# Kernel optimization log

Hardware: AMD Instinct MI355X
Metric: run time of the kernel (lower is better)

The kernel has to match this reference:

```python
import jax, jax.numpy as jnp
import numpy as np

B, S, D = 2, 2048, 2048
HQ, HKV, HD = 16, 8, 128
F = 8192
V = 32000
L = 2
SW = 512
SOFTCAP = 50.0
THETA = 10000.0
EPS = 1e-6
LAYER_TYPES = ("sliding_attention", "full_attention")
SCALE = HD ** -0.5


def _rms_norm(x, w):
    # Gemma-style RMSNorm: fp32 compute, (1 + weight) scale
    x32 = x.astype(jnp.float32)
    n = x32 * jax.lax.rsqrt(jnp.mean(x32 * x32, axis=-1, keepdims=True) + EPS)
    return (n * (1.0 + w.astype(jnp.float32))).astype(x.dtype)


def _rotate_half(x):
    x1, x2 = jnp.split(x, 2, axis=-1)
    return jnp.concatenate([-x2, x1], axis=-1)


def _rope_cos_sin(position_ids):
    inv_freq = 1.0 / (THETA ** (jnp.arange(0, HD, 2, dtype=jnp.float32) / HD))  # [HD/2]
    freqs = position_ids.astype(jnp.float32)[..., None] * inv_freq  # [B,S,HD/2]
    emb = jnp.concatenate([freqs, freqs], axis=-1)  # [B,S,HD]
    return jnp.cos(emb), jnp.sin(emb)


def _apply_rope(q, k, cos, sin):
    # q,k: [B,H,S,HD]; cos,sin: [B,S,HD] -> unsqueeze head dim
    c, s = cos[:, None], sin[:, None]
    return q * c + _rotate_half(q) * s, k * c + _rotate_half(k) * s


def _build_masks(attention_mask, position_ids):
    key_mask = attention_mask.astype(bool)  # [B,S]
    # segment ids from position resets (packed sequences)
    boundaries = (position_ids[:, 1:] <= position_ids[:, :-1]).astype(jnp.int32)
    seg = jnp.cumsum(jnp.concatenate([jnp.ones((B, 1), jnp.int32), boundaries], axis=1), axis=1)
    block = seg[:, :, None] == seg[:, None, :]  # [B,S,S]
    full = (key_mask[:, None, :] & block)[:, None]  # [B,1,S,S]
    rows = jnp.arange(S)
    dist = rows[:, None] - rows[None, :]
    left = (SW + 1) // 2
    right = SW // 2 + 1
    window = ((dist >= 0) & (dist < left)) | ((dist < 0) & (-dist < right))
    sliding = full & window[None, None]
    return {"full_attention": full, "sliding_attention": sliding}


def _attention(x, l, wq, wk, wv, wo, q_norm_w, k_norm_w, cos, sin, mask):
    q = jnp.einsum("bsd,dhe->bhse", x, wq[l].reshape(D, HQ, HD))
    k = jnp.einsum("bsd,dhe->bhse", x, wk[l].reshape(D, HKV, HD))
    v = jnp.einsum("bsd,dhe->bhse", x, wv[l].reshape(D, HKV, HD))
    q = _rms_norm(q, q_norm_w[l])
    k = _rms_norm(k, k_norm_w[l])
    q, k = _apply_rope(q, k, cos, sin)
    rep = HQ // HKV
    k = jnp.repeat(k, rep, axis=1)  # repeat_kv
    v = jnp.repeat(v, rep, axis=1)
    scores = jnp.einsum("bhqd,bhkd->bhqk", q, k) * SCALE
    scores = jnp.tanh(scores / SOFTCAP) * SOFTCAP  # logit softcapping
    big_neg = jnp.finfo(jnp.float32).min
    scores = jnp.where(mask, scores, big_neg)
    probs = jax.nn.softmax(scores.astype(jnp.float32), axis=-1).astype(x.dtype)
    out = jnp.einsum("bhqk,bhkd->bhqd", probs, v)
    out = out.transpose(0, 2, 1, 3).reshape(B, S, HQ * HD)
    return out @ wo[l]


def _mlp(x, l, w_gate_up, w_down):
    gu = x @ w_gate_up[l]
    gate, up = jnp.split(gu, 2, axis=-1)
    return (jax.nn.gelu(gate, approximate=True) * up) @ w_down[l]


def setup_inputs() -> dict:
    key = jax.random.key(0)
    ks = jax.random.split(key, 12)
    w = lambda k, shape: (jax.random.normal(k, shape, jnp.float32) * 0.02)
    inp = {
        "embed": w(ks[0], (V, D)),
        "wq": w(ks[1], (L, D, HQ * HD)),
        "wk": w(ks[2], (L, D, HKV * HD)),
        "wv": w(ks[3], (L, D, HKV * HD)),
        "wo": w(ks[4], (L, HQ * HD, D)),
        "q_norm_w": jnp.zeros((L, HD), jnp.float32),
        "k_norm_w": jnp.zeros((L, HD), jnp.float32),
        "ln_in": jnp.zeros((L, D), jnp.float32),
        "ln_post_attn": jnp.zeros((L, D), jnp.float32),
        "ln_pre_ffn": jnp.zeros((L, D), jnp.float32),
        "ln_post_ffn": jnp.zeros((L, D), jnp.float32),
        "w_gate_up": w(ks[5], (L, D, 2 * F)),
        "w_down": w(ks[6], (L, F, D)),
        "final_norm_w": jnp.zeros((D,), jnp.float32),
        "input_ids": jax.random.randint(ks[7], (B, S), 0, V, jnp.int32),
        "attention_mask": jnp.ones((B, S), jnp.int32),
        # packed sequences: positions reset at the midpoint of each row
        "position_ids": jnp.broadcast_to(
            jnp.concatenate([jnp.arange(S // 2), jnp.arange(S - S // 2)]).astype(jnp.int32)[None, :],
            (B, S),
        ),
    }
    return inp


def reference(embed, wq, wk, wv, wo, q_norm_w, k_norm_w, ln_in, ln_post_attn,
              ln_pre_ffn, ln_post_ffn, w_gate_up, w_down, final_norm_w,
              input_ids, attention_mask, position_ids):
    masks = _build_masks(attention_mask, position_ids)
    cos, sin = _rope_cos_sin(position_ids)
    # scaled word embedding (Gemma style)
    x = embed[input_ids] * jnp.asarray(D ** 0.5, embed.dtype)
    for l in range(L):
        mask = masks[LAYER_TYPES[l]]
        h = _rms_norm(x, ln_in[l])
        h = _attention(h, l, wq, wk, wv, wo, q_norm_w, k_norm_w, cos, sin, mask)
        x = x + _rms_norm(h, ln_post_attn[l])
        h = _rms_norm(x, ln_pre_ffn[l])
        h = _mlp(h, l, w_gate_up, w_down)
        x = x + _rms_norm(h, ln_post_ffn[l])
    return _rms_norm(x, final_norm_w)
```

## Files before the change

### kernel.cpp

```cpp
#include <hip/hip_runtime.h>
#include <cstdint>
#include <cstddef>

typedef __bf16 bf16x8 __attribute__((ext_vector_type(8)));
typedef float  f32x4  __attribute__((ext_vector_type(4)));

#define BATCH 2
#define SEQ   2048
#define DMODEL 2048
#define NHQ   16
#define NHKV  8
#define HDIM  128
#define FFDIM 8192
#define NTOK  4096

__device__ __forceinline__ f32x4 mfma16(bf16x8 a, bf16x8 b, f32x4 c) {
    return __builtin_amdgcn_mfma_f32_16x16x32_bf16(a, b, c, 0, 0, 0);
}

__device__ __forceinline__ void gload16(const __bf16* g, __bf16* l) {
    __builtin_amdgcn_global_load_lds(
        (const __attribute__((address_space(1))) void*)g,
        (__attribute__((address_space(3))) void*)l, 16, 0, 0);
}

__device__ inline float wave_sum64(float v) {
    v += __shfl_xor(v, 1);  v += __shfl_xor(v, 2);  v += __shfl_xor(v, 4);
    v += __shfl_xor(v, 8);  v += __shfl_xor(v, 16); v += __shfl_xor(v, 32);
    return v;
}

__device__ inline float block_sum256(float v, float* lds4) {
    v = wave_sum64(v);
    const int w = threadIdx.x >> 6;
    __syncthreads();
    if ((threadIdx.x & 63) == 0) lds4[w] = v;
    __syncthreads();
    return lds4[0] + lds4[1] + lds4[2] + lds4[3];
}

__device__ __forceinline__ float softcap_exp(float s_raw) {
    const float K1 = 0.08838834764831845f * 0.04f;
    float u = __expf(s_raw * K1);
    return __expf(50.f - 100.f * __builtin_amdgcn_rcpf(1.f + u));
}

__global__ void transpose_cvt(const float* __restrict__ src, __bf16* __restrict__ dst,
                              int K, int N) {
    __shared__ float tile[32][33];
    const int tx = threadIdx.x, ty = threadIdx.y;
    const int n0 = blockIdx.x * 32, k0 = blockIdx.y * 32;
    #pragma unroll
    for (int i = 0; i < 4; ++i)
        tile[ty + i * 8][tx] = src[(size_t)(k0 + ty + i * 8) * N + n0 + tx];
    __syncthreads();
    #pragma unroll
    for (int i = 0; i < 4; ++i)
        dst[(size_t)(n0 + ty + i * 8) * K + k0 + tx] = (__bf16)tile[tx][ty + i * 8];
}

__global__ void transpose_cvt_gu(const float* __restrict__ src, __bf16* __restrict__ dst,
                                 int K, int N) {
    __shared__ float tile[32][33];
    const int tx = threadIdx.x, ty = threadIdx.y;
    const int n0 = blockIdx.x * 32, k0 = blockIdx.y * 32;
    #pragma unroll
    for (int i = 0; i < 4; ++i)
        tile[ty + i * 8][tx] = src[(size_t)(k0 + ty + i * 8) * N + n0 + tx];
    __syncthreads();
    #pragma unroll
    for (int i = 0; i < 4; ++i) {
        int n = n0 + ty + i * 8;
        int rI;
        if (n < 8192) rI = ((n & ~15) << 1) + (n & 15);
        else { int u = n - 8192; rI = ((u & ~15) << 1) + 16 + (u & 15); }
        dst[(size_t)rI * K + k0 + tx] = (__bf16)tile[tx][ty + i * 8];
    }
}

__global__ void transpose_bf16_k(const __bf16* __restrict__ src0, __bf16* __restrict__ dst0,
                                 int R, int C) {
    __shared__ __bf16 tile[32][34];
    const int z = blockIdx.z;
    const __bf16* src = src0 + (size_t)z * R * C;
    __bf16* dst = dst0 + (size_t)z * R * C;
    const int tx = threadIdx.x, ty = threadIdx.y;
    const int c0 = blockIdx.x * 32, r0 = blockIdx.y * 32;
    #pragma unroll
    for (int i = 0; i < 4; ++i)
        tile[ty + i * 8][tx] = src[(size_t)(r0 + ty + i * 8) * C + c0 + tx];
    __syncthreads();
    #pragma unroll
    for (int i = 0; i < 4; ++i)
        dst[(size_t)(c0 + ty + i * 8) * R + r0 + tx] = tile[tx][ty + i * 8];
}

__global__ __launch_bounds__(256) void embed_k(const float* __restrict__ emb,
                                               const int* __restrict__ ids,
                                               float* __restrict__ x) {
    const int row = blockIdx.x, t = threadIdx.x;
    const int id = ids[row];
    const size_t src = (size_t)id * DMODEL, dst = (size_t)row * DMODEL;
    const float sc = 45.2548339959390f;
    float4 a = *(const float4*)&emb[src + t * 4];
    float4 b = *(const float4*)&emb[src + t * 4 + 1024];
    a.x *= sc; a.y *= sc; a.z *= sc; a.w *= sc;
    b.x *= sc; b.y *= sc; b.z *= sc; b.w *= sc;
    *(float4*)&x[dst + t * 4] = a;
    *(float4*)&x[dst + t * 4 + 1024] = b;
}

__global__ __launch_bounds__(256) void seg_scan(const int* __restrict__ pos,
                                                int* __restrict__ seg) {
    __shared__ int wsum[4];
    const int b = blockIdx.x, t = threadIdx.x;
    const int lane = t & 63, wv = t >> 6;
    const int base = b * SEQ;
    int f[8]; int loc = 0;
    #pragma unroll
    for (int i = 0; i < 8; ++i) {
        int s = t * 8 + i;
        int fl = (s > 0) ? (pos[base + s] <= pos[base + s - 1]) : 0;
        f[i] = fl; loc += fl;
    }
    int sc = loc;
    for (int o = 1; o < 64; o <<= 1) { int n = __shfl_up(sc, o); if (lane >= o) sc += n; }
    if (lane == 63) wsum[wv] = sc;
    __syncthreads();
    int wb = 0;
    for (int i = 0; i < wv; ++i) wb += wsum[i];
    int run = wb + sc - loc + 1;
    #pragma unroll
    for (int i = 0; i < 8; ++i) { run += f[i]; seg[base + t * 8 + i] = run; }
}

template<int MODE, int NH>
__global__ __launch_bounds__(256) void fused_norm_k(
        float* __restrict__ x, const float* __restrict__ hA, const float* __restrict__ hB,
        const float* __restrict__ wA, const float* __restrict__ wB,
        __bf16* __restrict__ outb, float* __restrict__ outf) {
    __shared__ float lds4[4];
    const int row = blockIdx.x, t = threadIdx.x;
    const size_t base = (size_t)row * DMODEL;
    const int c0 = t * 4, c1 = t * 4 + 1024;
    float v[8];
    if constexpr (MODE == 0) {
        float4 a = *(const float4*)&x[base + c0];
        float4 b = *(const float4*)&x[base + c1];
        v[0]=a.x; v[1]=a.y; v[2]=a.z; v[3]=a.w;
        v[4]=b.x; v[5]=b.y; v[6]=b.z; v[7]=b.w;
    } else {
        float4 ha = *(const float4*)&hA[base + c0];
        float4 hb = *(const float4*)&hA[base + c1];
        float hv[8] = {ha.x, ha.y, ha.z, ha.w, hb.x, hb.y, hb.z, hb.w};
        if constexpr (NH == 2) {
            float4 ga = *(const float4*)&hB[base + c0];
            float4 gb = *(const float4*)&hB[base + c1];
            hv[0]+=ga.x; hv[1]+=ga.y; hv[2]+=ga.z; hv[3]+=ga.w;
            hv[4]+=gb.x; hv[5]+=gb.y; hv[6]+=gb.z; hv[7]+=gb.w;
        }
        float ss = 0.f;
        #pragma unroll
        for (int i = 0; i < 8; ++i) ss += hv[i] * hv[i];
        float tot = block_sum256(ss, lds4);
        float rs = rsqrtf(tot * (1.f / DMODEL) + 1e-6f);
        float4 xa = *(const float4*)&x[base + c0];
        float4 xb = *(const float4*)&x[base + c1];
        float xv[8] = {xa.x, xa.y, xa.z, xa.w, xb.x, xb.y, xb.z, xb.w};
        #pragma unroll
        for (int i = 0; i < 8; ++i) {
            int c = (i < 4) ? c0 + i : c1 + i - 4;
            v[i] = xv[i] + hv[i] * rs * (1.f + wA[c]);
        }
        float4 o0 = {v[0], v[1], v[2], v[3]}, o1 = {v[4], v[5], v[6], v[7]};
        *(float4*)&x[base + c0] = o0;
        *(float4*)&x[base + c1] = o1;
    }
    float ss2 = 0.f;
    #pragma unroll
    for (int i = 0; i < 8; ++i) ss2 += v[i] * v[i];
    float tot2 = block_sum256(ss2, lds4);
    float rs2 = rsqrtf(tot2 * (1.f / DMODEL) + 1e-6f);
    #pragma unroll
    for (int i = 0; i < 8; ++i) {
        int c = (i < 4) ? c0 + i : c1 + i - 4;
        float o = v[i] * rs2 * (1.f + wB[c]);
        if constexpr (MODE == 2) outf[base + c] = o;
        else outb[base + c] = (__bf16)o;
    }
}

template<int MH, int NH>
__device__ __forceinline__ void quad(f32x4 (&acc)[8][4], const bf16x8 (&af)[4][2],
                                     const bf16x8 (&bfr)[2][2]) {
    #pragma unroll
    for (int mq = 0; mq < 4; ++mq)
        #pragma unroll
        for (int nq = 0; nq < 2; ++nq)
            #pragma unroll
            for (int ks = 0; ks < 2; ++ks)
                acc[MH*4+mq][NH*2+nq] = mfma16(af[mq][ks], bfr[nq][ks], acc[MH*4+mq][NH*2+nq]);
}

template<typename OutT, int GELU>
__global__ __launch_bounds__(512, 2) void gemm8p(const __bf16* __restrict__ A,
                                                 const __bf16* __restrict__ Bw,
                                                 OutT* __restrict__ C,
                                                 int M, int N, int Ksub, int lda, int ldb) {
    __shared__ __bf16 lds[65536];
    const int z = blockIdx.z;
    A += (size_t)z * Ksub;
    Bw += (size_t)z * Ksub;
    C += (size_t)z * M * N;

    const int nx = gridDim.x;
    const int ny = gridDim.y;
    const int nwg = nx * ny;
    const int orig = blockIdx.y * nx + blockIdx.x;
    const int wg = ((nwg & 7) == 0) ? ((orig & 7) * (nwg >> 3) + (orig >> 3)) : orig;
    const int gsize = 8 * nx;
    const int gid = wg / gsize;
    const int first_m = gid * 8;
    const int rows = min(8, ny - first_m);
    const int loc = wg - gid * gsize;
    const int bm = (first_m + loc % rows) * 256;
    const int bn = (loc / rows) * 256;

    const int t = threadIdx.x;
    const int w = t >> 6, lane = t & 63;
    const int wm = w >> 2, wn = w & 3;
    const int lg = lane >> 4, lr = lane & 15;

    const int rS = t >> 3, sS = t & 7;
    const int colS = ((sS ^ (rS & 7)) << 3);
    const __bf16* Ag = A + (size_t)(bm + rS) * lda + colS;
    const __bf16* Bg = Bw + (size_t)(bn + rS) * ldb + colS;
    const int nt = Ksub >> 6;

#define STAGE_A(kt, h) { \
        const __bf16* g_ = Ag + (size_t)(h) * 128 * lda + (size_t)(kt) * 64; \
        const int li_ = (((kt) & 1) << 15) + ((h) << 13) + t * 8; \
        gload16(g_, &lds[li_]); \
        gload16(g_ + (size_t)64 * lda, &lds[li_ + 4096]); }
#define STAGE_B(kt, h) { \
        const __bf16* g_ = Bg + (size_t)(h) * 128 * ldb + (size_t)(kt) * 64; \
        const int li_ = (((kt) & 1) << 15) + 16384 + ((h) << 13) + t * 8; \
        gload16(g_, &lds[li_]); \
        gload16(g_ + (size_t)64 * ldb, &lds[li_ + 4096]); }
#define STAGE_T(kt) { STAGE_A(kt, 0); STAGE_A(kt, 1); STAGE_B(kt, 0); STAGE_B(kt, 1); }

    f32x4 acc[8][4] = {};
    bf16x8 af[4][2], bf0[2][2], bf1[2][2];

    const int swz = (lr & 7) << 3;
    const int aBase = wm * 8192;
    const int bBase = 16384 + (wn >> 1) * 8192;
    const int bRow0 = (wn & 1) * 64;

    STAGE_T(0);
    if (nt > 1) {
        STAGE_T(1);
        asm volatile("s_waitcnt vmcnt(8)" ::: "memory");
    } else {
        asm volatile("s_waitcnt vmcnt(0)" ::: "memory");
    }
    __builtin_amdgcn_s_barrier();
    asm volatile("" ::: "memory");

    for (int kt = 0; kt < nt; ++kt) {
        const int buf = (kt & 1) << 15;
        const bool p1 = (kt + 1 < nt), p2 = (kt + 2 < nt);
        #pragma unroll
        for (int mq = 0; mq < 4; ++mq)
            #pragma unroll
            for (int ks = 0; ks < 2; ++ks)
                af[mq][ks] = *(const bf16x8*)&lds[buf + aBase + (((mq*16 + lr)*64 + ks*32 + lg*8) ^ swz)];
        #pragma unroll
        for (int nq = 0; nq < 2; ++nq)
            #pragma unroll
            for (int ks = 0; ks < 2; ++ks)
                bf0[nq][ks] = *(const bf16x8*)&lds[buf + bBase + (((bRow0 + nq*16 + lr)*64 + ks*32 + lg*8) ^ swz)];
        __builtin_amdgcn_sched_barrier(0);
        __builtin_amdgcn_s_barrier();
        asm volatile("s_waitcnt lgkmcnt(0)" ::: "memory");
        __builtin_amdgcn_sched_barrier(0);
        __builtin_amdgcn_s_setprio(1);
        quad<0,0>(acc, af, bf0);
        __builtin_amdgcn_s_setprio(0);
        __builtin_amdgcn_s_barrier();
        asm volatile("" ::: "memory");
        #pragma unroll
        for (int nq = 0; nq < 2; ++nq)
            #pragma unroll
            for (int ks = 0; ks < 2; ++ks)
                bf1[nq][ks] = *(const bf16x8*)&lds[buf + bBase + (((bRow0 + 32 + nq*16 + lr)*64 + ks*32 + lg*8) ^ swz)];
        __builtin_amdgcn_sched_barrier(0);
        __builtin_amdgcn_s_barrier();
        asm volatile("s_waitcnt lgkmcnt(0)" ::: "memory");
        __builtin_amdgcn_sched_barrier(0);
        __builtin_amdgcn_s_setprio(1);
        quad<0,1>(acc, af, bf1);
        __builtin_amdgcn_s_setprio(0);
        __builtin_amdgcn_s_barrier();
        asm volatile("" ::: "memory");
        #pragma unroll
        for (int mq = 0; mq < 4; ++mq)
            #pragma unroll
            for (int ks = 0; ks < 2; ++ks)
                af[mq][ks] = *(const bf16x8*)&lds[buf + aBase + (((64 + mq*16 + lr)*64 + ks*32 + lg*8) ^ swz)];
        __builtin_amdgcn_sched_barrier(0);
        __builtin_amdgcn_s_barrier();
        asm volatile("s_waitcnt lgkmcnt(0)" ::: "memory");
        __builtin_amdgcn_sched_barrier(0);
        __builtin_amdgcn_s_setprio(1);
        quad<1,1>(acc, af, bf1);
        __builtin_amdgcn_s_setprio(0);
        __builtin_amdgcn_s_barrier();
        asm volatile("" ::: "memory");
        if (p2) {
            STAGE_T(kt + 2);
            asm volatile("s_waitcnt vmcnt(8)" ::: "memory");
        } else if (p1) {
            asm volatile("s_waitcnt vmcnt(0)" ::: "memory");
        }
        __builtin_amdgcn_s_barrier();
        __builtin_amdgcn_sched_barrier(0);
        __builtin_amdgcn_s_setprio(1);
        quad<1,0>(acc, af, bf0);
        __builtin_amdgcn_s_setprio(0);
        __builtin_amdgcn_s_barrier();
        asm volatile("" ::: "memory");
    }
#undef STAGE_A
#undef STAGE_B
#undef STAGE_T

    if constexpr (GELU) {
        const int nhalf = N >> 1;
        #pragma unroll
        for (int m = 0; m < 8; ++m)
            #pragma unroll
            for (int pp = 0; pp < 2; ++pp)
                #pragma unroll
                for (int r = 0; r < 4; ++r) {
                    float g = acc[m][2 * pp][r];
                    float u = acc[m][2 * pp + 1][r];
                    float a2 = 1.5957691216057308f * (g + 0.044715f * g * g * g);
                    float sig = __builtin_amdgcn_rcpf(1.f + __expf(-a2));
                    float res = g * sig * u;
                    const int row = bm + wm * 128 + m * 16 + lg * 4 + r;
                    const int col = (bn >> 1) + wn * 32 + pp * 16 + lr;
                    C[(size_t)row * nhalf + col] = (OutT)res;
                }
    } else {
        #pragma unroll
        for (int m = 0; m < 8; ++m)
            #pragma unroll
            for (int n = 0; n < 4; ++n)
                #pragma unroll
                for (int r = 0; r < 4; ++r) {
                    const int row = bm + wm * 128 + m * 16 + lg * 4 + r;
                    const int col = bn + wn * 64 + n * 16 + lr;
                    C[(size_t)row * N + col] = (OutT)acc[m][n][r];
                }
    }
}

__global__ __launch_bounds__(256) void qkv_post(const __bf16* __restrict__ qkv,
                                                const float* __restrict__ qnw,
                                                const float* __restrict__ knw,
                                                const int* __restrict__ posid,
                                                __bf16* __restrict__ qg,
                                                __bf16* __restrict__ kg,
                                                __bf16* __restrict__ vg) {
    const int slot = blockIdx.x * 4 + (threadIdx.x >> 6);
    const int lane = threadIdx.x & 63;
    const int token = slot >> 5, j = slot & 31;
    const int b = token >> 11, s = token & (SEQ - 1);
    int base;
    const float* nw = nullptr;
    if (j < 16)      { base = j * 128;                nw = qnw; }
    else if (j < 24) { base = 2048 + (j - 16) * 128;  nw = knw; }
    else             { base = 3072 + (j - 24) * 128; }
    float e0 = (float)qkv[(size_t)token * 4096 + base + lane];
    float e1 = (float)qkv[(size_t)token * 4096 + base + lane + 64];
    if (j < 24) {
        float ss = wave_sum64(e0 * e0 + e1 * e1);
        float rs = rsqrtf(ss * (1.f / 128.f) + 1e-6f);
        e0 *= rs * (1.f + nw[lane]);
        e1 *= rs * (1.f + nw[lane + 64]);
        float p = (float)posid[token];
        float inv = exp2f(-13.287712379549449f * ((float)lane * (1.f / 64.f)));
        float f = p * inv;
        float c = cosf(f), sn = sinf(f);
        float o0 = e0 * c - e1 * sn;
        float o1 = e1 * c + e0 * sn;
        e0 = o0; e1 = o1;
    }
    size_t dst; __bf16* out;
    if (j < 16)      { dst = ((size_t)(b * NHQ  + j)        * SEQ + s) * HDIM; out = qg; }
    else if (j < 24) { dst = ((size_t)(b * NHKV + (j - 16)) * SEQ + s) * HDIM; out = kg; }
    else             { dst = ((size_t)(b * NHKV + (j - 24)) * SEQ + s) * HDIM; out = vg; }
    out[dst + lane] = (__bf16)e0;
    out[dst + lane + 64] = (__bf16)e1;
}

template<int SLIDING>
__global__ __launch_bounds__(256, 2) void attn_k(const __bf16* __restrict__ qg,
                                                 const __bf16* __restrict__ kg,
                                                 const __bf16* __restrict__ vtg,
                                                 const int* __restrict__ seg,
                                                 const int* __restrict__ amask,
                                                 __bf16* __restrict__ outg) {
    __shared__ __align__(16) __bf16 Ks[64][136];
    __shared__ __align__(16) __bf16 Vs[128][72];
    __shared__ __align__(16) __bf16 Ps[4][16][72];
    __shared__ int segq_s[64], segk_s[64], kmk_s[64];
    __shared__ int flag_s;
    const int bh = blockIdx.y;
    const int b = bh >> 4, h = bh & 15, kvh = h >> 1;
    const int qb = blockIdx.x * 64;
    const int t = threadIdx.x, w = t >> 6, lane = t & 63;
    const int lg = lane >> 4, lr = lane & 15;
    const int segbase = b * SEQ;

    const size_t qoff = ((size_t)(b * NHQ + h) * SEQ + qb + w * 16) * HDIM;
    bf16x8 qf[4];
    #pragma unroll
    for (int kk = 0; kk < 4; ++kk)
        qf[kk] = *(const bf16x8*)&qg[qoff + (size_t)lr * HDIM + kk * 32 + lg * 8];
    if (t < 64) segq_s[t] = seg[segbase + qb + t];

    const int sqmin = seg[segbase + qb], sqmax = seg[segbase + qb + 63];

    const int krow = t >> 4, kcol = (t & 15) * 8;
    const int vrow = t >> 3, vcol = (t & 7) * 8;
    const __bf16* kB = kg + ((size_t)(b * NHKV + kvh) * SEQ) * HDIM + (size_t)krow * HDIM + kcol;
    const __bf16* vB = vtg + ((size_t)(b * NHKV + kvh) * HDIM + vrow) * SEQ + vcol;

    auto chunk_active = [&](int kb) -> bool {
        if (SLIDING && (qb - kb < -318 || qb - kb > 319)) return false;
        int skmin = seg[segbase + kb], skmax = seg[segbase + kb + 63];
        return (skmax >= sqmin) && (skmin <= sqmax);
    };
    auto next_kb = [&](int kb) -> int {
        for (kb += 64; kb < SEQ; kb += 64)
            if (chunk_active(kb)) return kb;
        return SEQ;
    };

    int4 kr0, kr1, kr2, kr3, vr0, vr1, vr2, vr3;
#define LOADR(kb_) { \
        kr0 = *(const int4*)(kB + (size_t)(kb_) * HDIM); \
        kr1 = *(const int4*)(kB + (size_t)((kb_) + 16) * HDIM); \
        kr2 = *(const int4*)(kB + (size_t)((kb_) + 32) * HDIM); \
        kr3 = *(const int4*)(kB + (size_t)((kb_) + 48) * HDIM); \
        vr0 = *(const int4*)(vB + (kb_)); \
        vr1 = *(const int4*)(vB + (size_t)32 * SEQ + (kb_)); \
        vr2 = *(const int4*)(vB + (size_t)64 * SEQ + (kb_)); \
        vr3 = *(const int4*)(vB + (size_t)96 * SEQ + (kb_)); }

    f32x4 oacc[8] = {};
    float den[4] = {0.f, 0.f, 0.f, 0.f};

    int kb = chunk_active(0) ? 0 : next_kb(0);
    if (kb < SEQ) LOADR(kb);

    while (kb < SEQ) {
        const int nkb = next_kb(kb);
        __syncthreads();
        *(int4*)&Ks[krow     ][kcol] = kr0;
        *(int4*)&Ks[krow + 16][kcol] = kr1;
        *(int4*)&Ks[krow + 32][kcol] = kr2;
        *(int4*)&Ks[krow + 48][kcol] = kr3;
        *(int4*)&Vs[vrow     ][vcol] = vr0;
        *(int4*)&Vs[vrow + 32][vcol] = vr1;
        *(int4*)&Vs[vrow + 64][vcol] = vr2;
        *(int4*)&Vs[vrow + 96][vcol] = vr3;
        if (w == 0) {
            int m = amask[segbase + kb + lane];
            int sk = seg[segbase + kb + lane];
            kmk_s[lane] = m; segk_s[lane] = sk;
            bool allm = (__ballot(m != 0) == ~0ull);
            bool segu = __all(sk == sqmin) && (sqmin == sqmax);
            bool wall = !SLIDING || (qb - kb >= -193 && qb - kb <= 192);
            if (lane == 0) flag_s = (allm && segu && wall) ? 1 : 0;
        }
        __syncthreads();
        if (nkb < SEQ) LOADR(nkb);
        const bool fast = (flag_s != 0);

        #pragma unroll
        for (int n = 0; n < 4; ++n) {
            f32x4 sc = {};
            #pragma unroll
            for (int kk = 0; kk < 4; ++kk) {
                bf16x8 bfr = *(const bf16x8*)&Ks[n * 16 + lr][kk * 32 + lg * 8];
                sc = mfma16(qf[kk], bfr, sc);
            }
            if (fast) {
                #pragma unroll
                for (int r = 0; r < 4; ++r) {
                    int row = lg * 4 + r;
                    float p = softcap_exp(sc[r]);
                    den[r] += p;
                    Ps[w][row][n * 16 + lr] = (__bf16)p;
                }
            } else {
                #pragma unroll
                for (int r = 0; r < 4; ++r) {
                    int row = lg * 4 + r;
                    int qi = qb + w * 16 + row;
                    int ki = kb + n * 16 + lr;
                    bool ok = (kmk_s[n * 16 + lr] != 0) &&
                              (segq_s[w * 16 + row] == segk_s[n * 16 + lr]);
                    if (SLIDING) { int d = qi - ki; ok = ok && (d >= -256) && (d <= 255); }
                    float p = ok ? softcap_exp(sc[r]) : 0.f;
                    den[r] += p;
                    Ps[w][row][n * 16 + lr] = (__bf16)p;
                }
            }
        }
        #pragma unroll
        for (int kk2 = 0; kk2 < 2; ++kk2) {
            bf16x8 pf = *(const bf16x8*)&Ps[w][lr][kk2 * 32 + lg * 8];
            #pragma unroll
            for (int n2 = 0; n2 < 8; ++n2) {
                bf16x8 vf = *(const bf16x8*)&Vs[n2 * 16 + lr][kk2 * 32 + lg * 8];
                oacc[n2] = mfma16(pf, vf, oacc[n2]);
            }
        }
        kb = nkb;
    }
#undef LOADR
    #pragma unroll
    for (int r = 0; r < 4; ++r) {
        float v = den[r];
        v += __shfl_xor(v, 1); v += __shfl_xor(v, 2);
        v += __shfl_xor(v, 4); v += __shfl_xor(v, 8);
        den[r] = __builtin_amdgcn_rcpf(v);
    }
    #pragma unroll
    for (int n2 = 0; n2 < 8; ++n2)
        #pragma unroll
        for (int r = 0; r < 4; ++r) {
            int row = qb + w * 16 + lg * 4 + r;
            float val = oacc[n2][r] * den[r];
            outg[((size_t)(b * SEQ) + row) * DMODEL + h * HDIM + n2 * 16 + lr] = (__bf16)val;
        }
}

extern "C" void kernel_launch(void* const* d_in, const int* in_sizes, int n_in,
                              void* d_out, int out_size, void* d_ws, size_t ws_size,
                              hipStream_t stream) {
    const float* embedw = (const float*)d_in[0];
    const float* wq   = (const float*)d_in[1];
    const float* wk   = (const float*)d_in[2];
    const float* wv   = (const float*)d_in[3];
    const float* wo   = (const float*)d_in[4];
    const float* qnw  = (const float*)d_in[5];
    const float* knw  = (const float*)d_in[6];
    const float* lnin = (const float*)d_in[7];
    const float* lnpa = (const float*)d_in[8];
    const float* lnpf = (const float*)d_in[9];
    const float* lnpff= (const float*)d_in[10];
    const float* wguW = (const float*)d_in[11];
    const float* wdnW = (const float*)d_in[12];
    const float* fnw  = (const float*)d_in[13];
    const int* ids    = (const int*)d_in[14];
    const int* amask  = (const int*)d_in[15];
    const int* posid  = (const int*)d_in[16];
    float* outp = (float*)d_out;

    char* ws = (char*)d_ws;
    size_t off = 0;
    auto A = [&](size_t b) -> char* {
        char* p = ws + off;
        off = (off + b + 255) & ~(size_t)255;
        return p;
    };
    __bf16* qkvwt = (__bf16*)A((size_t)4096 * 2048 * 2);
    __bf16* wot   = (__bf16*)A((size_t)2048 * 2048 * 2);
    __bf16* wgut  = (__bf16*)A((size_t)16384 * 2048 * 2);
    __bf16* wdnt  = (__bf16*)A((size_t)2048 * 8192 * 2);
    float*  x     = (float*)A((size_t)NTOK * DMODEL * 4);
    __bf16* hbuf  = (__bf16*)A((size_t)NTOK * DMODEL * 2);
    __bf16* qkvb  = (__bf16*)A((size_t)NTOK * 4096 * 2);
    __bf16* qbh   = (__bf16*)A((size_t)BATCH * NHQ  * SEQ * HDIM * 2);
    __bf16* kbh   = (__bf16*)A((size_t)BATCH * NHKV * SEQ * HDIM * 2);
    __bf16* vbh   = (__bf16*)A((size_t)BATCH * NHKV * SEQ * HDIM * 2);
    __bf16* vtbh  = (__bf16*)A((size_t)BATCH * NHKV * SEQ * HDIM * 2);
    __bf16* attnb = (__bf16*)A((size_t)NTOK * DMODEL * 2);
    __bf16* actb  = (__bf16*)A((size_t)NTOK * FFDIM * 2);
    float*  pbuf  = (float*)A((size_t)2 * NTOK * DMODEL * 4);
    int*    seg   = (int*)A((size_t)BATCH * SEQ * 4);
    if (off > ws_size) return;

    const dim3 tb(32, 8);
    seg_scan<<<BATCH, 256, 0, stream>>>(posid, seg);
    embed_k<<<NTOK, 256, 0, stream>>>(embedw, ids, x);
    fused_norm_k<0,1><<<NTOK, 256, 0, stream>>>(x, nullptr, nullptr, nullptr, lnin, hbuf, nullptr);

    for (int l = 0; l < 2; ++l) {
        transpose_cvt<<<dim3(64, 64), tb, 0, stream>>>(wq + (size_t)l * 2048 * 2048,
            qkvwt, 2048, 2048);
        transpose_cvt<<<dim3(32, 64), tb, 0, stream>>>(wk + (size_t)l * 2048 * 1024,
            qkvwt + (size_t)2048 * 2048, 2048, 1024);
        transpose_cvt<<<dim3(32, 64), tb, 0, stream>>>(wv + (size_t)l * 2048 * 1024,
            qkvwt + (size_t)3072 * 2048, 2048, 1024);
        transpose_cvt<<<dim3(64, 64), tb, 0, stream>>>(wo + (size_t)l * 2048 * 2048,
            wot, 2048, 2048);
        transpose_cvt_gu<<<dim3(512, 64), tb, 0, stream>>>(wguW + (size_t)l * 2048 * 16384,
            wgut, 2048, 16384);
        transpose_cvt<<<dim3(64, 256), tb, 0, stream>>>(wdnW + (size_t)l * 8192 * 2048,
            wdnt, 8192, 2048);

        gemm8p<__bf16,0><<<dim3(16, 16, 1), 512, 0, stream>>>(hbuf, qkvwt, qkvb,
                                                              4096, 4096, 2048, 2048, 2048);
        qkv_post<<<32768, 256, 0, stream>>>(qkvb, qnw + l * 128, knw + l * 128, posid,
                                            qbh, kbh, vbh);
        transpose_bf16_k<<<dim3(4, 64, BATCH * NHKV), tb, 0, stream>>>(vbh, vtbh, SEQ, HDIM);
        if (l == 0)
            attn_k<1><<<dim3(SEQ / 64, BATCH * NHQ), 256, 0, stream>>>(qbh, kbh, vtbh, seg,
                                                                       amask, attnb);
        else
            attn_k<0><<<dim3(SEQ / 64, BATCH * NHQ), 256, 0, stream>>>(qbh, kbh, vtbh, seg,
                                                                       amask, attnb);
        gemm8p<float,0><<<dim3(8, 16, 2), 512, 0, stream>>>(attnb, wot, pbuf,
                                                            4096, 2048, 1024, 2048, 2048);
        fused_norm_k<1,2><<<NTOK, 256, 0, stream>>>(x, pbuf, pbuf + (size_t)NTOK * DMODEL,
                                                    lnpa + l * 2048, lnpf + l * 2048,
                                                    hbuf, nullptr);
        gemm8p<__bf16,1><<<dim3(64, 16, 1), 512, 0, stream>>>(hbuf, wgut, actb,
                                                              4096, 16384, 2048, 2048, 2048);
        gemm8p<float,0><<<dim3(8, 16, 2), 512, 0, stream>>>(actb, wdnt, pbuf,
                                                            4096, 2048, 4096, 8192, 8192);
        if (l == 0)
            fused_norm_k<1,2><<<NTOK, 256, 0, stream>>>(x, pbuf, pbuf + (size_t)NTOK * DMODEL,
                                                        lnpff, lnin + 2048, hbuf, nullptr);
        else
            fused_norm_k<2,2><<<NTOK, 256, 0, stream>>>(x, pbuf, pbuf + (size_t)NTOK * DMODEL,
                                                        lnpff + 2048, fnw, nullptr, outp);
    }
}
```

Baseline: 1.493 ms.

## Software-pipeline LDS fragment reads and split global staging in GEMM loop

The GEMM main loop now loads the next iteration's A and B0 fragments from LDS at the end of the current iteration. It issues the B1 and second-half A reads while MFMA quads are running, using partial lgkmcnt waits instead of a full barrier before each read. Global-to-LDS staging for tile kt+2 is split so the A half is issued earlier than the B half, and swizzle offsets are hoisted out of the loop. The aim is to hide LDS latency and cut barrier stalls. The cost is more live registers and more delicate buffer-reuse ordering.

Result: faster. 1.458 ms (-2.3%).

```diff
diff --git a/kernel.cpp b/kernel.cpp
--- a/kernel.cpp
+++ b/kernel.cpp
@@ -247,7 +247,6 @@
         const int li_ = (((kt) & 1) << 15) + 16384 + ((h) << 13) + t * 8; \
         gload16(g_, &lds[li_]); \
         gload16(g_ + (size_t)64 * ldb, &lds[li_ + 4096]); }
-#define STAGE_T(kt) { STAGE_A(kt, 0); STAGE_A(kt, 1); STAGE_B(kt, 0); STAGE_B(kt, 1); }
 
     f32x4 acc[8][4] = {};
     bf16x8 af[4][2], bf0[2][2], bf1[2][2];
@@ -256,61 +255,63 @@
     const int aBase = wm * 8192;
     const int bBase = 16384 + (wn >> 1) * 8192;
     const int bRow0 = (wn & 1) * 64;
-
-    STAGE_T(0);
+    const int lo0 = (lg * 8) ^ swz;
+    const int lo1 = (32 + lg * 8) ^ swz;
+
+#define RD_A(bufv, rowoff) { \
+        _Pragma("unroll") \
+        for (int mq = 0; mq < 4; ++mq) { \
+            const int rb_ = (bufv) + aBase + ((rowoff) + mq * 16 + lr) * 64; \
+            af[mq][0] = *(const bf16x8*)&lds[rb_ + lo0]; \
+            af[mq][1] = *(const bf16x8*)&lds[rb_ + lo1]; } }
+#define RD_B0(bufv) { \
+        _Pragma("unroll") \
+        for (int nq = 0; nq < 2; ++nq) { \
+            const int rb_ = (bufv) + bBase + (bRow0 + nq * 16 + lr) * 64; \
+            bf0[nq][0] = *(const bf16x8*)&lds[rb_ + lo0]; \
+            bf0[nq][1] = *(const bf16x8*)&lds[rb_ + lo1]; } }
+#define RD_B1(bufv) { \
+        _Pragma("unroll") \
+        for (int nq = 0; nq < 2; ++nq) { \
+            const int rb_ = (bufv) + bBase + (bRow0 + 32 + nq * 16 + lr) * 64; \
+            bf1[nq][0] = *(const bf16x8*)&lds[rb_ + lo0]; \
+            bf1[nq][1] = *(const bf16x8*)&lds[rb_ + lo1]; } }
+
+    STAGE_A(0, 0); STAGE_A(0, 1); STAGE_B(0, 0); STAGE_B(0, 1);
     if (nt > 1) {
-        STAGE_T(1);
+        STAGE_A(1, 0); STAGE_A(1, 1); STAGE_B(1, 0); STAGE_B(1, 1);
         asm volatile("s_waitcnt vmcnt(8)" ::: "memory");
     } else {
         asm volatile("s_waitcnt vmcnt(0)" ::: "memory");
     }
     __builtin_amdgcn_s_barrier();
     asm volatile("" ::: "memory");
+    RD_A(0, 0);
+    RD_B0(0);
 
     for (int kt = 0; kt < nt; ++kt) {
         const int buf = (kt & 1) << 15;
+        const int obuf = buf ^ (1 << 15);
         const bool p1 = (kt + 1 < nt), p2 = (kt + 2 < nt);
-        #pragma unroll
-        for (int mq = 0; mq < 4; ++mq)
-            #pragma unroll
-            for (int ks = 0; ks < 2; ++ks)
-                af[mq][ks] = *(const bf16x8*)&lds[buf + aBase + (((mq*16 + lr)*64 + ks*32 + lg*8) ^ swz)];
-        #pragma unroll
-        for (int nq = 0; nq < 2; ++nq)
-            #pragma unroll
-            for (int ks = 0; ks < 2; ++ks)
-                bf0[nq][ks] = *(const bf16x8*)&lds[buf + bBase + (((bRow0 + nq*16 + lr)*64 + ks*32 + lg*8) ^ swz)];
-        __builtin_amdgcn_sched_barrier(0);
-        __builtin_amdgcn_s_barrier();
-        asm volatile("s_waitcnt lgkmcnt(0)" ::: "memory");
+        RD_B1(buf);
+        asm volatile("s_waitcnt lgkmcnt(4)" ::: "memory");
         __builtin_amdgcn_sched_barrier(0);
         __builtin_amdgcn_s_setprio(1);
         quad<0,0>(acc, af, bf0);
         __builtin_amdgcn_s_setprio(0);
         __builtin_amdgcn_s_barrier();
         asm volatile("" ::: "memory");
-        #pragma unroll
-        for (int nq = 0; nq < 2; ++nq)
-            #pragma unroll
-            for (int ks = 0; ks < 2; ++ks)
-                bf1[nq][ks] = *(const bf16x8*)&lds[buf + bBase + (((bRow0 + 32 + nq*16 + lr)*64 + ks*32 + lg*8) ^ swz)];
-        __builtin_amdgcn_sched_barrier(0);
-        __builtin_amdgcn_s_barrier();
         asm volatile("s_waitcnt lgkmcnt(0)" ::: "memory");
         __builtin_amdgcn_sched_barrier(0);
         __builtin_amdgcn_s_setprio(1);
         quad<0,1>(acc, af, bf1);
         __builtin_amdgcn_s_setprio(0);
+        __builtin_amdgcn_sched_barrier(0);
+        RD_A(buf, 64);
+        asm volatile("s_waitcnt lgkmcnt(0)" ::: "memory");
         __builtin_amdgcn_s_barrier();
         asm volatile("" ::: "memory");
-        #pragma unroll
-        for (int mq = 0; mq < 4; ++mq)
-            #pragma unroll
-            for (int ks = 0; ks < 2; ++ks)
-                af[mq][ks] = *(const bf16x8*)&lds[buf + aBase + (((64 + mq*16 + lr)*64 + ks*32 + lg*8) ^ swz)];
-        __builtin_amdgcn_sched_barrier(0);
-        __builtin_amdgcn_s_barrier();
-        asm volatile("s_waitcnt lgkmcnt(0)" ::: "memory");
+        if (p2) { STAGE_A(kt + 2, 0); STAGE_A(kt + 2, 1); }
         __builtin_amdgcn_sched_barrier(0);
         __builtin_amdgcn_s_setprio(1);
         quad<1,1>(acc, af, bf1);
@@ -318,22 +319,27 @@
         __builtin_amdgcn_s_barrier();
         asm volatile("" ::: "memory");
         if (p2) {
-            STAGE_T(kt + 2);
+            STAGE_B(kt + 2, 0); STAGE_B(kt + 2, 1);
             asm volatile("s_waitcnt vmcnt(8)" ::: "memory");
         } else if (p1) {
             asm volatile("s_waitcnt vmcnt(0)" ::: "memory");
         }
         __builtin_amdgcn_s_barrier();
+        asm volatile("" ::: "memory");
         __builtin_amdgcn_sched_barrier(0);
         __builtin_amdgcn_s_setprio(1);
         quad<1,0>(acc, af, bf0);
         __builtin_amdgcn_s_setprio(0);
+        __builtin_amdgcn_sched_barrier(0);
+        if (p1) { RD_A(obuf, 0); RD_B0(obuf); }
         __builtin_amdgcn_s_barrier();
         asm volatile("" ::: "memory");
     }
 #undef STAGE_A
 #undef STAGE_B
-#undef STAGE_T
+#undef RD_A
+#undef RD_B0
+#undef RD_B1
 
     if constexpr (GELU) {
         const int nhalf = N >> 1;
```
